# Optimization experiments

Hardware: AMD Instinct MI355X
Metric: run time of the kernel (lower is better)

The kernel has to match this reference:

```python
import jax, jax.numpy as jnp
import numpy as np

USER = 100000
ITEM = 200000
LATDIM = 128
GNN_LAYER = 3
UUGNN_LAYER = 2
N_EDGES = 600000
UU_EDGES = 300000


def setup_inputs() -> dict:
    key = jax.random.key(0)
    ks = jax.random.split(key, 8)
    N = USER + ITEM
    return {
        "uEmbeds0": jax.random.normal(ks[0], (USER, LATDIM), dtype=jnp.float32) * 0.05,
        "iEmbeds0": jax.random.normal(ks[1], (ITEM, LATDIM), dtype=jnp.float32) * 0.05,
        "adj_rows": jax.random.randint(ks[2], (N_EDGES,), 0, N, dtype=jnp.int32),
        "adj_cols": jax.random.randint(ks[3], (N_EDGES,), 0, N, dtype=jnp.int32),
        "adj_vals": jax.random.uniform(ks[4], (N_EDGES,), dtype=jnp.float32),
        "uadj_rows": jax.random.randint(ks[5], (UU_EDGES,), 0, USER, dtype=jnp.int32),
        "uadj_cols": jax.random.randint(ks[6], (UU_EDGES,), 0, USER, dtype=jnp.int32),
        "uadj_vals": jax.random.uniform(ks[7], (UU_EDGES,), dtype=jnp.float32),
    }


def _spmm(rows, cols, vals, x, n_rows):
    # out[r] = sum_{e: rows[e]==r} vals[e] * x[cols[e]]  (COO sparse @ dense)
    return jax.ops.segment_sum(vals[:, None] * x[cols], rows, num_segments=n_rows)


def reference(uEmbeds0, iEmbeds0, adj_rows, adj_cols, adj_vals,
              uadj_rows, uadj_cols, uadj_vals):
    N = USER + ITEM
    # LightGCN over bipartite adjacency, pool='sum' over layer-0..L embeddings
    # (dropout in eval mode -> identity)
    embeds = jnp.concatenate([uEmbeds0, iEmbeds0], axis=0)  # [N, d]
    acc = embeds
    for _ in range(GNN_LAYER):
        embeds = _spmm(adj_rows, adj_cols, adj_vals, embeds, N)
        acc = acc + embeds
    ui_uEmbed = acc[:USER]
    ui_iEmbed = acc[USER:]

    # LightGCN2 over user-user adjacency, sum of layer embeddings
    ulat = uEmbeds0
    uacc = ulat
    for _ in range(UUGNN_LAYER):
        ulat = _spmm(uadj_rows, uadj_cols, uadj_vals, ulat, USER)
        uacc = uacc + ulat
    return (ui_uEmbed, ui_iEmbed, uacc)
```

## Files before the change

### kernel.cpp

```cpp
#include <hip/hip_runtime.h>
#include <hip/hip_fp16.h>

#define USER_N   100000
#define ITEM_N   200000
#define LATDIM   128
#define NV4      32
#define NV8      16
#define N_TOTAL  300000
#define NR_ALL   400000
#define N_EDGES_C  600000
#define UU_EDGES_C 300000
#define NE_ALL   900000
#define SCAN_B   256
#define CONV_T   (N_TOTAL * NV8)

struct alignas(16) h8 { __half2 a, b, c, d; };
struct alignas(8)  Edge { int c; float v; };

typedef float f4_ext __attribute__((ext_vector_type(4)));
typedef int   i4_ext __attribute__((ext_vector_type(4)));
typedef int   i2_ext __attribute__((ext_vector_type(2)));

union H8I { i4_ext i; h8 h; };
union EDI { i2_ext i; Edge e; };

__device__ __forceinline__ float4 nt_load4(const float4* p) {
    f4_ext v = __builtin_nontemporal_load((const f4_ext*)p);
    return make_float4(v.x, v.y, v.z, v.w);
}
__device__ __forceinline__ void nt_store4(float4* p, float4 a) {
    f4_ext v = {a.x, a.y, a.z, a.w};
    __builtin_nontemporal_store(v, (f4_ext*)p);
}
__device__ __forceinline__ h8 nt_load_h8(const h8* p) {
    H8I u; u.i = __builtin_nontemporal_load((const i4_ext*)p);
    return u.h;
}
__device__ __forceinline__ Edge nt_load_edge(const Edge* p) {
    EDI u; u.i = __builtin_nontemporal_load((const i2_ext*)p);
    return u.e;
}

__device__ __forceinline__ h8 to_h8(float4 lo, float4 hi) {
    h8 r;
    r.a = __floats2half2_rn(lo.x, lo.y); r.b = __floats2half2_rn(lo.z, lo.w);
    r.c = __floats2half2_rn(hi.x, hi.y); r.d = __floats2half2_rn(hi.z, hi.w);
    return r;
}
__device__ __forceinline__ void h8_to_f(h8 h, float4& lo, float4& hi) {
    float2 p = __half22float2(h.a), q = __half22float2(h.b);
    float2 s = __half22float2(h.c), t = __half22float2(h.d);
    lo = make_float4(p.x, p.y, q.x, q.y);
    hi = make_float4(s.x, s.y, t.x, t.y);
}
__device__ __forceinline__ void fma4(float4& a, float v, float4 x) {
    a.x += v * x.x; a.y += v * x.y; a.z += v * x.z; a.w += v * x.w;
}
__device__ __forceinline__ float4 add4(float4 a, float4 b) {
    return make_float4(a.x + b.x, a.y + b.y, a.z + b.z, a.w + b.w);
}

__global__ void conv_hist_kernel(const float4* __restrict__ uE,
                                 const float4* __restrict__ iE,
                                 h8* __restrict__ E16,
                                 const int* __restrict__ ar,
                                 const int* __restrict__ ur,
                                 int* __restrict__ cnt) {
    int t = blockIdx.x * blockDim.x + threadIdx.x;
    if (t < CONV_T) {
        int f4i = t * 2;
        const int ub = USER_N * NV4;
        float4 lo, hi;
        if (f4i < ub) { lo = nt_load4(uE + f4i);        hi = nt_load4(uE + f4i + 1); }
        else          { lo = nt_load4(iE + (f4i - ub)); hi = nt_load4(iE + (f4i - ub) + 1); }
        E16[t] = to_h8(lo, hi);
    } else {
        int i = t - CONV_T;
        if (i < N_EDGES_C)   atomicAdd(&cnt[ar[i]], 1);
        else if (i < NE_ALL) atomicAdd(&cnt[ur[i - N_EDGES_C] + N_TOTAL], 1);
    }
}

__global__ void scan_block_kernel(const int* __restrict__ cnt,
                                  int* __restrict__ rptr,
                                  int* __restrict__ bsum, int n) {
    __shared__ int s[SCAN_B];
    int i = blockIdx.x * SCAN_B + threadIdx.x;
    int v = (i < n) ? cnt[i] : 0;
    s[threadIdx.x] = v;
    __syncthreads();
    for (int off = 1; off < SCAN_B; off <<= 1) {
        int t = (threadIdx.x >= off) ? s[threadIdx.x - off] : 0;
        __syncthreads();
        s[threadIdx.x] += t;
        __syncthreads();
    }
    if (i < n) rptr[i] = s[threadIdx.x] - v;
    if (threadIdx.x == SCAN_B - 1) bsum[blockIdx.x] = s[threadIdx.x];
}

__global__ void scan_bsum_kernel(int* __restrict__ bsum, int nb) {
    __shared__ int s[SCAN_B];
    __shared__ int carry;
    if (threadIdx.x == 0) carry = 0;
    __syncthreads();
    for (int base = 0; base < nb; base += SCAN_B) {
        int i = base + threadIdx.x;
        int v = (i < nb) ? bsum[i] : 0;
        s[threadIdx.x] = v;
        __syncthreads();
        for (int off = 1; off < SCAN_B; off <<= 1) {
            int t = (threadIdx.x >= off) ? s[threadIdx.x - off] : 0;
            __syncthreads();
            s[threadIdx.x] += t;
            __syncthreads();
        }
        if (i < nb) bsum[i] = s[threadIdx.x] - v + carry;
        __syncthreads();
        if (threadIdx.x == 0) carry += s[SCAN_B - 1];
        __syncthreads();
    }
}

__global__ void scan_add_kernel(int* __restrict__ rptr, const int* __restrict__ bsum,
                                int* __restrict__ cursor, int n, int n_edges) {
    int i = blockIdx.x * blockDim.x + threadIdx.x;
    if (i < n) {
        int v = rptr[i] + bsum[i / SCAN_B];
        rptr[i]   = v;
        cursor[i] = v;
    }
    if (i == 0) rptr[n] = n_edges;
}

__global__ void scatter2_kernel(const int* __restrict__ ar, const int* __restrict__ ac,
                                const float* __restrict__ av,
                                const int* __restrict__ ur, const int* __restrict__ uc,
                                const float* __restrict__ uv,
                                int* __restrict__ cursor,
                                Edge* __restrict__ edges) {
    int i = blockIdx.x * blockDim.x + threadIdx.x;
    int r; Edge ed;
    if (i < N_EDGES_C)      { r = ar[i];             ed.c = ac[i];           ed.v = av[i]; }
    else if (i < NE_ALL)    { int j = i - N_EDGES_C; r = ur[j] + N_TOTAL; ed.c = uc[j] + N_TOTAL; ed.v = uv[j]; }
    else return;
    int pos = atomicAdd(&cursor[r], 1);
    edges[pos] = ed;
}

__device__ __forceinline__ int e16_row(int c) {
    return (c < N_TOTAL) ? c : c - N_TOTAL;
}

__global__ void spmm_pass1(const int* __restrict__ rptr,
                           const Edge* __restrict__ edges,
                           const h8* __restrict__ E16,
                           h8* __restrict__ cur1) {
    int t = blockIdx.x * blockDim.x + threadIdx.x;
    int r = t >> 4, sub = t & 15;
    if (r >= NR_ALL) return;
    int e0 = rptr[r], e1 = rptr[r + 1];

    float4 a0l = make_float4(0,0,0,0), a0h = a0l, a1l = a0l, a1h = a0l;
    int e = e0;
    for (; e + 2 <= e1; e += 2) {
        Edge d0 = edges[e], d1 = edges[e + 1];
        h8 h0 = E16[(size_t)e16_row(d0.c) * NV8 + sub];
        h8 h1 = E16[(size_t)e16_row(d1.c) * NV8 + sub];
        float4 lo, hi;
        h8_to_f(h0, lo, hi); fma4(a0l, d0.v, lo); fma4(a0h, d0.v, hi);
        h8_to_f(h1, lo, hi); fma4(a1l, d1.v, lo); fma4(a1h, d1.v, hi);
    }
    if (e < e1) {
        Edge d0 = edges[e];
        h8 h0 = E16[(size_t)e16_row(d0.c) * NV8 + sub];
        float4 lo, hi;
        h8_to_f(h0, lo, hi); fma4(a0l, d0.v, lo); fma4(a0h, d0.v, hi);
    }
    cur1[(size_t)r * NV8 + sub] = to_h8(add4(a0l, a1l), add4(a0h, a1h));
}

__global__ void spmm_pass2(const int* __restrict__ rptr,
                           const Edge* __restrict__ edges,
                           const h8* __restrict__ cur1,
                           const h8* __restrict__ E16,
                           h8* __restrict__ cur2,
                           float4* __restrict__ uacc) {
    int t = blockIdx.x * blockDim.x + threadIdx.x;
    int r = t >> 4, sub = t & 15;
    if (r >= NR_ALL) return;
    int e0 = rptr[r], e1 = rptr[r + 1];

    float4 a0l = make_float4(0,0,0,0), a0h = a0l, a1l = a0l, a1h = a0l;
    int e = e0;
    for (; e + 2 <= e1; e += 2) {
        Edge d0 = edges[e], d1 = edges[e + 1];
        h8 h0 = cur1[(size_t)d0.c * NV8 + sub];
        h8 h1 = cur1[(size_t)d1.c * NV8 + sub];
        float4 lo, hi;
        h8_to_f(h0, lo, hi); fma4(a0l, d0.v, lo); fma4(a0h, d0.v, hi);
        h8_to_f(h1, lo, hi); fma4(a1l, d1.v, lo); fma4(a1h, d1.v, hi);
    }
    if (e < e1) {
        Edge d0 = edges[e];
        h8 h0 = cur1[(size_t)d0.c * NV8 + sub];
        float4 lo, hi;
        h8_to_f(h0, lo, hi); fma4(a0l, d0.v, lo); fma4(a0h, d0.v, hi);
    }
    float4 al = add4(a0l, a1l), ah = add4(a0h, a1h);

    size_t o = (size_t)r * NV8 + sub;
    if (r < N_TOTAL) {
        cur2[o] = to_h8(al, ah);
    } else {
        int ur = r - N_TOTAL;
        float4 u0l, u0h, l1l, l1h;
        h8_to_f(E16[(size_t)ur * NV8 + sub], u0l, u0h);
        h8_to_f(cur1[o], l1l, l1h);
        size_t of4 = (size_t)ur * NV4 + sub * 2;
        nt_store4(uacc + of4,     add4(add4(u0l, l1l), al));
        nt_store4(uacc + of4 + 1, add4(add4(u0h, l1h), ah));
    }
}

__global__ void spmm_pass3(const int* __restrict__ rptr,
                           const Edge* __restrict__ edges,
                           const h8* __restrict__ cur2,
                           const h8* __restrict__ cur1,
                           const h8* __restrict__ E16,
                           float4* __restrict__ acc) {
    int t = blockIdx.x * blockDim.x + threadIdx.x;
    int r = t >> 4, sub = t & 15;
    if (r >= N_TOTAL) return;
    int e0 = rptr[r], e1 = rptr[r + 1];

    float4 a0l = make_float4(0,0,0,0), a0h = a0l, a1l = a0l, a1h = a0l;
    int e = e0;
    for (; e + 2 <= e1; e += 2) {
        Edge d0 = nt_load_edge(edges + e), d1 = nt_load_edge(edges + e + 1);
        h8 h0 = cur2[(size_t)d0.c * NV8 + sub];
        h8 h1 = cur2[(size_t)d1.c * NV8 + sub];
        float4 lo, hi;
        h8_to_f(h0, lo, hi); fma4(a0l, d0.v, lo); fma4(a0h, d0.v, hi);
        h8_to_f(h1, lo, hi); fma4(a1l, d1.v, lo); fma4(a1h, d1.v, hi);
    }
    if (e < e1) {
        Edge d0 = nt_load_edge(edges + e);
        h8 h0 = cur2[(size_t)d0.c * NV8 + sub];
        float4 lo, hi;
        h8_to_f(h0, lo, hi); fma4(a0l, d0.v, lo); fma4(a0h, d0.v, hi);
    }
    float4 al = add4(a0l, a1l), ah = add4(a0h, a1h);

    size_t o = (size_t)r * NV8 + sub;
    float4 ezl, ezh, l1l, l1h, l2l, l2h;
    h8_to_f(nt_load_h8(E16 + o),  ezl, ezh);
    h8_to_f(nt_load_h8(cur1 + o), l1l, l1h);
    h8_to_f(cur2[o], l2l, l2h);

    size_t of4 = (size_t)r * NV4 + sub * 2;
    nt_store4(acc + of4,     add4(add4(ezl, l1l), add4(l2l, al)));
    nt_store4(acc + of4 + 1, add4(add4(ezh, l1h), add4(l2h, ah)));
}

extern "C" void kernel_launch(void* const* d_in, const int* in_sizes, int n_in,
                              void* d_out, int out_size, void* d_ws, size_t ws_size,
                              hipStream_t stream) {
    const float* uE    = (const float*)d_in[0];
    const float* iE    = (const float*)d_in[1];
    const int*   arows = (const int*)  d_in[2];
    const int*   acols = (const int*)  d_in[3];
    const float* avals = (const float*)d_in[4];
    const int*   urows = (const int*)  d_in[5];
    const int*   ucols = (const int*)  d_in[6];
    const float* uvals = (const float*)d_in[7];

    float* acc  = (float*)d_out;
    float* uacc = acc + (size_t)N_TOTAL * LATDIM;

    h8*    E16  = (h8*)d_ws;
    h8*    cur1 = E16 + (size_t)N_TOTAL * NV8;
    h8*    cur2 = cur1 + (size_t)NR_ALL * NV8;
    int*   cnt  = (int*)(cur2 + (size_t)N_TOTAL * NV8);
    int*   rptr = cnt + NR_ALL;
    int*   curp = rptr + NR_ALL + 1;
    int*   bsum = curp + NR_ALL;
    Edge*  edges = (Edge*)(bsum + 4096);

    const int TB = 256;

    hipMemsetAsync(cnt, 0, NR_ALL * sizeof(int), stream);
    {
        int threads = CONV_T + NE_ALL;
        conv_hist_kernel<<<(threads + TB - 1) / TB, TB, 0, stream>>>(
            (const float4*)uE, (const float4*)iE, E16, arows, urows, cnt);
    }
    {
        int nb = (NR_ALL + SCAN_B - 1) / SCAN_B;
        scan_block_kernel<<<nb, SCAN_B, 0, stream>>>(cnt, rptr, bsum, NR_ALL);
        scan_bsum_kernel<<<1, SCAN_B, 0, stream>>>(bsum, nb);
        scan_add_kernel<<<(NR_ALL + TB - 1) / TB, TB, 0, stream>>>(
            rptr, bsum, curp, NR_ALL, NE_ALL);
    }
    scatter2_kernel<<<(NE_ALL + TB - 1) / TB, TB, 0, stream>>>(
        arows, acols, avals, urows, ucols, uvals, curp, edges);

    {
        int threads = NR_ALL * NV8;
        int grid = (threads + TB - 1) / TB;
        spmm_pass1<<<grid, TB, 0, stream>>>(rptr, edges, E16, cur1);
        spmm_pass2<<<grid, TB, 0, stream>>>(rptr, edges, cur1, E16,
                                            cur2, (float4*)uacc);
    }
    {
        int threads = N_TOTAL * NV8;
        int grid = (threads + TB - 1) / TB;
        spmm_pass3<<<grid, TB, 0, stream>>>(rptr, edges, cur2, cur1, E16,
                                            (float4*)acc);
    }
}
```

Measured before the change: 352.8 us.

## Split fp32-to-fp16 conversion across hist, scan and scatter kernels

The embedding conversion to fp16 is divided into four chunks, and each chunk runs as extra blocks appended to the histogram, block-scan, scan-add and scatter kernels. This fills the latency-bound, low-occupancy CSR-build kernels with bandwidth work instead of doing all conversion up front. The spmm pass1 output store also becomes nontemporal. The cost is more complex kernels whose extra blocks may slow the critical atomic and scan phases.

```diff
diff --git a/kernel.cpp b/kernel.cpp
--- a/kernel.cpp
+++ b/kernel.cpp
@@ -13,6 +13,10 @@
 #define NE_ALL   900000
 #define SCAN_B   256
 #define CONV_T   (N_TOTAL * NV8)
+#define CONV_BLK 4688
+#define CONV_CS  (CONV_BLK * 256)
+#define HIST_BLK ((NE_ALL + 255) / 256)
+#define SCANB_BLK ((NR_ALL + SCAN_B - 1) / SCAN_B)
 
 struct alignas(16) h8 { __half2 a, b, c, d; };
 struct alignas(8)  Edge { int c; float v; };
@@ -35,6 +39,10 @@
 __device__ __forceinline__ h8 nt_load_h8(const h8* p) {
     H8I u; u.i = __builtin_nontemporal_load((const i4_ext*)p);
     return u.h;
+}
+__device__ __forceinline__ void nt_store_h8(h8* p, h8 v) {
+    H8I u; u.h = v;
+    __builtin_nontemporal_store(u.i, (i4_ext*)p);
 }
 __device__ __forceinline__ Edge nt_load_edge(const Edge* p) {
     EDI u; u.i = __builtin_nontemporal_load((const i2_ext*)p);
@@ -60,43 +68,53 @@
     return make_float4(a.x + b.x, a.y + b.y, a.z + b.z, a.w + b.w);
 }
 
-__global__ void conv_hist_kernel(const float4* __restrict__ uE,
-                                 const float4* __restrict__ iE,
-                                 h8* __restrict__ E16,
-                                 const int* __restrict__ ar,
-                                 const int* __restrict__ ur,
-                                 int* __restrict__ cnt) {
-    int t = blockIdx.x * blockDim.x + threadIdx.x;
-    if (t < CONV_T) {
-        int f4i = t * 2;
-        const int ub = USER_N * NV4;
-        float4 lo, hi;
-        if (f4i < ub) { lo = nt_load4(uE + f4i);        hi = nt_load4(uE + f4i + 1); }
-        else          { lo = nt_load4(iE + (f4i - ub)); hi = nt_load4(iE + (f4i - ub) + 1); }
-        E16[t] = to_h8(lo, hi);
-    } else {
-        int i = t - CONV_T;
+__device__ __forceinline__ void conv_do(int t, const float4* __restrict__ uE,
+                                        const float4* __restrict__ iE,
+                                        h8* __restrict__ E16) {
+    if (t < 0 || t >= CONV_T) return;
+    int f4i = t * 2;
+    const int ub = USER_N * NV4;
+    float4 lo, hi;
+    if (f4i < ub) { lo = nt_load4(uE + f4i);        hi = nt_load4(uE + f4i + 1); }
+    else          { lo = nt_load4(iE + (f4i - ub)); hi = nt_load4(iE + (f4i - ub) + 1); }
+    E16[t] = to_h8(lo, hi);
+}
+
+__global__ void hist_convA(const int* __restrict__ ar, const int* __restrict__ ur,
+                           int* __restrict__ cnt,
+                           const float4* __restrict__ uE, const float4* __restrict__ iE,
+                           h8* __restrict__ E16) {
+    if (blockIdx.x < HIST_BLK) {
+        int i = blockIdx.x * blockDim.x + threadIdx.x;
         if (i < N_EDGES_C)   atomicAdd(&cnt[ar[i]], 1);
         else if (i < NE_ALL) atomicAdd(&cnt[ur[i - N_EDGES_C] + N_TOTAL], 1);
-    }
-}
-
-__global__ void scan_block_kernel(const int* __restrict__ cnt,
-                                  int* __restrict__ rptr,
-                                  int* __restrict__ bsum, int n) {
-    __shared__ int s[SCAN_B];
-    int i = blockIdx.x * SCAN_B + threadIdx.x;
-    int v = (i < n) ? cnt[i] : 0;
-    s[threadIdx.x] = v;
-    __syncthreads();
-    for (int off = 1; off < SCAN_B; off <<= 1) {
-        int t = (threadIdx.x >= off) ? s[threadIdx.x - off] : 0;
+    } else {
+        conv_do((blockIdx.x - HIST_BLK) * 256 + (int)threadIdx.x, uE, iE, E16);
+    }
+}
+
+__global__ void scanblock_convB(const int* __restrict__ cnt,
+                                int* __restrict__ rptr, int* __restrict__ bsum,
+                                const float4* __restrict__ uE, const float4* __restrict__ iE,
+                                h8* __restrict__ E16) {
+    if (blockIdx.x < SCANB_BLK) {
+        __shared__ int s[SCAN_B];
+        int i = blockIdx.x * SCAN_B + threadIdx.x;
+        int v = (i < NR_ALL) ? cnt[i] : 0;
+        s[threadIdx.x] = v;
         __syncthreads();
-        s[threadIdx.x] += t;
-        __syncthreads();
-    }
-    if (i < n) rptr[i] = s[threadIdx.x] - v;
-    if (threadIdx.x == SCAN_B - 1) bsum[blockIdx.x] = s[threadIdx.x];
+        for (int off = 1; off < SCAN_B; off <<= 1) {
+            int t = (threadIdx.x >= off) ? s[threadIdx.x - off] : 0;
+            __syncthreads();
+            s[threadIdx.x] += t;
+            __syncthreads();
+        }
+        if (i < NR_ALL) rptr[i] = s[threadIdx.x] - v;
+        if (threadIdx.x == SCAN_B - 1) bsum[blockIdx.x] = s[threadIdx.x];
+    } else {
+        conv_do((blockIdx.x - SCANB_BLK) * 256 + (int)threadIdx.x + CONV_CS,
+                uE, iE, E16);
+    }
 }
 
 __global__ void scan_bsum_kernel(int* __restrict__ bsum, int nb) {
@@ -122,30 +140,43 @@
     }
 }
 
-__global__ void scan_add_kernel(int* __restrict__ rptr, const int* __restrict__ bsum,
-                                int* __restrict__ cursor, int n, int n_edges) {
-    int i = blockIdx.x * blockDim.x + threadIdx.x;
-    if (i < n) {
-        int v = rptr[i] + bsum[i / SCAN_B];
-        rptr[i]   = v;
-        cursor[i] = v;
-    }
-    if (i == 0) rptr[n] = n_edges;
-}
-
-__global__ void scatter2_kernel(const int* __restrict__ ar, const int* __restrict__ ac,
-                                const float* __restrict__ av,
-                                const int* __restrict__ ur, const int* __restrict__ uc,
-                                const float* __restrict__ uv,
-                                int* __restrict__ cursor,
-                                Edge* __restrict__ edges) {
-    int i = blockIdx.x * blockDim.x + threadIdx.x;
-    int r; Edge ed;
-    if (i < N_EDGES_C)      { r = ar[i];             ed.c = ac[i];           ed.v = av[i]; }
-    else if (i < NE_ALL)    { int j = i - N_EDGES_C; r = ur[j] + N_TOTAL; ed.c = uc[j] + N_TOTAL; ed.v = uv[j]; }
-    else return;
-    int pos = atomicAdd(&cursor[r], 1);
-    edges[pos] = ed;
+__global__ void scanadd_convC(int* __restrict__ rptr, const int* __restrict__ bsum,
+                              int* __restrict__ cursor,
+                              const float4* __restrict__ uE, const float4* __restrict__ iE,
+                              h8* __restrict__ E16) {
+    if (blockIdx.x < SCANB_BLK) {
+        int i = blockIdx.x * blockDim.x + threadIdx.x;
+        if (i < NR_ALL) {
+            int v = rptr[i] + bsum[i / SCAN_B];
+            rptr[i]   = v;
+            cursor[i] = v;
+        }
+        if (i == 0) rptr[NR_ALL] = NE_ALL;
+    } else {
+        conv_do((blockIdx.x - SCANB_BLK) * 256 + (int)threadIdx.x + 2 * CONV_CS,
+                uE, iE, E16);
+    }
+}
+
+__global__ void scatter_convD(const int* __restrict__ ar, const int* __restrict__ ac,
+                              const float* __restrict__ av,
+                              const int* __restrict__ ur, const int* __restrict__ uc,
+                              const float* __restrict__ uv,
+                              int* __restrict__ cursor, Edge* __restrict__ edges,
+                              const float4* __restrict__ uE, const float4* __restrict__ iE,
+                              h8* __restrict__ E16) {
+    if (blockIdx.x < HIST_BLK) {
+        int i = blockIdx.x * blockDim.x + threadIdx.x;
+        int r; Edge ed;
+        if (i < N_EDGES_C)   { r = ar[i];             ed.c = ac[i];           ed.v = av[i]; }
+        else if (i < NE_ALL) { int j = i - N_EDGES_C; r = ur[j] + N_TOTAL; ed.c = uc[j] + N_TOTAL; ed.v = uv[j]; }
+        else return;
+        int pos = atomicAdd(&cursor[r], 1);
+        edges[pos] = ed;
+    } else {
+        conv_do((blockIdx.x - HIST_BLK) * 256 + (int)threadIdx.x + 3 * CONV_CS,
+                uE, iE, E16);
+    }
 }
 
 __device__ __forceinline__ int e16_row(int c) {
@@ -177,7 +208,7 @@
         float4 lo, hi;
         h8_to_f(h0, lo, hi); fma4(a0l, d0.v, lo); fma4(a0h, d0.v, hi);
     }
-    cur1[(size_t)r * NV8 + sub] = to_h8(add4(a0l, a1l), add4(a0h, a1h));
+    nt_store_h8(cur1 + (size_t)r * NV8 + sub, to_h8(add4(a0l, a1l), add4(a0h, a1h)));
 }
 
 __global__ void spmm_pass2(const int* __restrict__ rptr,
@@ -288,22 +319,17 @@
     Edge*  edges = (Edge*)(bsum + 4096);
 
     const int TB = 256;
+    const float4* uE4 = (const float4*)uE;
+    const float4* iE4 = (const float4*)iE;
 
     hipMemsetAsync(cnt, 0, NR_ALL * sizeof(int), stream);
-    {
-        int threads = CONV_T + NE_ALL;
-        conv_hist_kernel<<<(threads + TB - 1) / TB, TB, 0, stream>>>(
-            (const float4*)uE, (const float4*)iE, E16, arows, urows, cnt);
-    }
-    {
-        int nb = (NR_ALL + SCAN_B - 1) / SCAN_B;
-        scan_block_kernel<<<nb, SCAN_B, 0, stream>>>(cnt, rptr, bsum, NR_ALL);
-        scan_bsum_kernel<<<1, SCAN_B, 0, stream>>>(bsum, nb);
-        scan_add_kernel<<<(NR_ALL + TB - 1) / TB, TB, 0, stream>>>(
-            rptr, bsum, curp, NR_ALL, NE_ALL);
-    }
-    scatter2_kernel<<<(NE_ALL + TB - 1) / TB, TB, 0, stream>>>(
-        arows, acols, avals, urows, ucols, uvals, curp, edges);
+
+    hist_convA<<<HIST_BLK + CONV_BLK, TB, 0, stream>>>(arows, urows, cnt, uE4, iE4, E16);
+    scanblock_convB<<<SCANB_BLK + CONV_BLK, SCAN_B, 0, stream>>>(cnt, rptr, bsum, uE4, iE4, E16);
+    scan_bsum_kernel<<<1, SCAN_B, 0, stream>>>(bsum, SCANB_BLK);
+    scanadd_convC<<<SCANB_BLK + CONV_BLK, TB, 0, stream>>>(rptr, bsum, curp, uE4, iE4, E16);
+    scatter_convD<<<HIST_BLK + CONV_BLK, TB, 0, stream>>>(
+        arows, acols, avals, urows, ucols, uvals, curp, edges, uE4, iE4, E16);
 
     {
         int threads = NR_ALL * NV8;
```

Result: slower. 364.4 us (+3.3%).

## Fuse CSR build and fp16 conversion into one cooperative kernel

Applied to the files above, without the earlier changes.

Replaces the memset, histogram/convert, three scan kernels and scatter kernel with a single cooperative kernel that uses grid-wide syncs between phases. The fp16 embedding conversion is split into quarters and interleaved with the histogram, block scan and bsum scan phases so that otherwise idle blocks have bandwidth work to do. This removes several kernel launches and their gaps. In exchange it adds five grid barriers, caps the grid at 1024 blocks with grid-stride loops, and depends on co-residency being possible under the launch bounds.

```diff
diff --git a/kernel.cpp b/kernel.cpp
--- a/kernel.cpp
+++ b/kernel.cpp
@@ -1,5 +1,8 @@
 #include <hip/hip_runtime.h>
 #include <hip/hip_fp16.h>
+#include <hip/hip_cooperative_groups.h>
+
+namespace cg = cooperative_groups;
 
 #define USER_N   100000
 #define ITEM_N   200000
@@ -13,6 +16,9 @@
 #define NE_ALL   900000
 #define SCAN_B   256
 #define CONV_T   (N_TOTAL * NV8)
+#define CONV_Q   (CONV_T / 4)
+#define NCH      ((NR_ALL + SCAN_B - 1) / SCAN_B)
+#define COOP_BLK 1024
 
 struct alignas(16) h8 { __half2 a, b, c, d; };
 struct alignas(8)  Edge { int c; float v; };
@@ -60,92 +66,105 @@
     return make_float4(a.x + b.x, a.y + b.y, a.z + b.z, a.w + b.w);
 }
 
-__global__ void conv_hist_kernel(const float4* __restrict__ uE,
-                                 const float4* __restrict__ iE,
-                                 h8* __restrict__ E16,
-                                 const int* __restrict__ ar,
-                                 const int* __restrict__ ur,
-                                 int* __restrict__ cnt) {
-    int t = blockIdx.x * blockDim.x + threadIdx.x;
-    if (t < CONV_T) {
-        int f4i = t * 2;
-        const int ub = USER_N * NV4;
-        float4 lo, hi;
-        if (f4i < ub) { lo = nt_load4(uE + f4i);        hi = nt_load4(uE + f4i + 1); }
-        else          { lo = nt_load4(iE + (f4i - ub)); hi = nt_load4(iE + (f4i - ub) + 1); }
-        E16[t] = to_h8(lo, hi);
-    } else {
-        int i = t - CONV_T;
-        if (i < N_EDGES_C)   atomicAdd(&cnt[ar[i]], 1);
-        else if (i < NE_ALL) atomicAdd(&cnt[ur[i - N_EDGES_C] + N_TOTAL], 1);
-    }
-}
-
-__global__ void scan_block_kernel(const int* __restrict__ cnt,
-                                  int* __restrict__ rptr,
-                                  int* __restrict__ bsum, int n) {
-    __shared__ int s[SCAN_B];
-    int i = blockIdx.x * SCAN_B + threadIdx.x;
-    int v = (i < n) ? cnt[i] : 0;
-    s[threadIdx.x] = v;
-    __syncthreads();
-    for (int off = 1; off < SCAN_B; off <<= 1) {
-        int t = (threadIdx.x >= off) ? s[threadIdx.x - off] : 0;
-        __syncthreads();
-        s[threadIdx.x] += t;
-        __syncthreads();
-    }
-    if (i < n) rptr[i] = s[threadIdx.x] - v;
-    if (threadIdx.x == SCAN_B - 1) bsum[blockIdx.x] = s[threadIdx.x];
-}
-
-__global__ void scan_bsum_kernel(int* __restrict__ bsum, int nb) {
+__device__ __forceinline__ void conv_do(int t, const float4* __restrict__ uE,
+                                        const float4* __restrict__ iE,
+                                        h8* __restrict__ E16) {
+    if (t < 0 || t >= CONV_T) return;
+    int f4i = t * 2;
+    const int ub = USER_N * NV4;
+    float4 lo, hi;
+    if (f4i < ub) { lo = nt_load4(uE + f4i);        hi = nt_load4(uE + f4i + 1); }
+    else          { lo = nt_load4(iE + (f4i - ub)); hi = nt_load4(iE + (f4i - ub) + 1); }
+    E16[t] = to_h8(lo, hi);
+}
+
+__global__ void __launch_bounds__(256, 4)
+csr_conv_coop(const float4* __restrict__ uE, const float4* __restrict__ iE,
+              h8* __restrict__ E16,
+              const int* __restrict__ ar, const int* __restrict__ ac,
+              const float* __restrict__ av,
+              const int* __restrict__ ur, const int* __restrict__ uc,
+              const float* __restrict__ uv,
+              int* __restrict__ cnt, int* __restrict__ rptr,
+              int* __restrict__ cursor, int* __restrict__ bsum,
+              Edge* __restrict__ edges) {
+    cg::grid_group grid = cg::this_grid();
     __shared__ int s[SCAN_B];
     __shared__ int carry;
-    if (threadIdx.x == 0) carry = 0;
-    __syncthreads();
-    for (int base = 0; base < nb; base += SCAN_B) {
-        int i = base + threadIdx.x;
-        int v = (i < nb) ? bsum[i] : 0;
+
+    const int NT  = COOP_BLK * 256;
+    const int tid = blockIdx.x * blockDim.x + threadIdx.x;
+
+    for (int i = tid; i < NR_ALL; i += NT) cnt[i] = 0;
+    for (int t = tid; t < CONV_Q; t += NT) conv_do(t, uE, iE, E16);
+    grid.sync();
+
+    for (int i = tid; i < NE_ALL; i += NT) {
+        if (i < N_EDGES_C) atomicAdd(&cnt[ar[i]], 1);
+        else               atomicAdd(&cnt[ur[i - N_EDGES_C] + N_TOTAL], 1);
+    }
+    for (int t = CONV_Q + tid; t < 2 * CONV_Q; t += NT) conv_do(t, uE, iE, E16);
+    grid.sync();
+
+    for (int ch = blockIdx.x; ch < NCH; ch += gridDim.x) {
+        int i = ch * SCAN_B + threadIdx.x;
+        int v = (i < NR_ALL) ? cnt[i] : 0;
         s[threadIdx.x] = v;
         __syncthreads();
         for (int off = 1; off < SCAN_B; off <<= 1) {
-            int t = (threadIdx.x >= off) ? s[threadIdx.x - off] : 0;
-            __syncthreads();
-            s[threadIdx.x] += t;
+            int t2 = (threadIdx.x >= off) ? s[threadIdx.x - off] : 0;
+            __syncthreads();
+            s[threadIdx.x] += t2;
             __syncthreads();
         }
-        if (i < nb) bsum[i] = s[threadIdx.x] - v + carry;
+        if (i < NR_ALL) rptr[i] = s[threadIdx.x] - v;
+        if (threadIdx.x == SCAN_B - 1) bsum[ch] = s[threadIdx.x];
         __syncthreads();
-        if (threadIdx.x == 0) carry += s[SCAN_B - 1];
+    }
+    for (int t = 2 * CONV_Q + tid; t < 3 * CONV_Q; t += NT) conv_do(t, uE, iE, E16);
+    grid.sync();
+
+    if (blockIdx.x == 0) {
+        if (threadIdx.x == 0) carry = 0;
         __syncthreads();
-    }
-}
-
-__global__ void scan_add_kernel(int* __restrict__ rptr, const int* __restrict__ bsum,
-                                int* __restrict__ cursor, int n, int n_edges) {
-    int i = blockIdx.x * blockDim.x + threadIdx.x;
-    if (i < n) {
+        for (int base = 0; base < NCH; base += SCAN_B) {
+            int i = base + threadIdx.x;
+            int v = (i < NCH) ? bsum[i] : 0;
+            s[threadIdx.x] = v;
+            __syncthreads();
+            for (int off = 1; off < SCAN_B; off <<= 1) {
+                int t2 = (threadIdx.x >= off) ? s[threadIdx.x - off] : 0;
+                __syncthreads();
+                s[threadIdx.x] += t2;
+                __syncthreads();
+            }
+            if (i < NCH) bsum[i] = s[threadIdx.x] - v + carry;
+            __syncthreads();
+            if (threadIdx.x == 0) carry += s[SCAN_B - 1];
+            __syncthreads();
+        }
+    } else {
+        int t = 3 * CONV_Q + (blockIdx.x - 1) * 256 + (int)threadIdx.x;
+        int stride = (COOP_BLK - 1) * 256;
+        for (; t < CONV_T; t += stride) conv_do(t, uE, iE, E16);
+    }
+    grid.sync();
+
+    for (int i = tid; i < NR_ALL; i += NT) {
         int v = rptr[i] + bsum[i / SCAN_B];
         rptr[i]   = v;
         cursor[i] = v;
     }
-    if (i == 0) rptr[n] = n_edges;
-}
-
-__global__ void scatter2_kernel(const int* __restrict__ ar, const int* __restrict__ ac,
-                                const float* __restrict__ av,
-                                const int* __restrict__ ur, const int* __restrict__ uc,
-                                const float* __restrict__ uv,
-                                int* __restrict__ cursor,
-                                Edge* __restrict__ edges) {
-    int i = blockIdx.x * blockDim.x + threadIdx.x;
-    int r; Edge ed;
-    if (i < N_EDGES_C)      { r = ar[i];             ed.c = ac[i];           ed.v = av[i]; }
-    else if (i < NE_ALL)    { int j = i - N_EDGES_C; r = ur[j] + N_TOTAL; ed.c = uc[j] + N_TOTAL; ed.v = uv[j]; }
-    else return;
-    int pos = atomicAdd(&cursor[r], 1);
-    edges[pos] = ed;
+    if (tid == 0) rptr[NR_ALL] = NE_ALL;
+    grid.sync();
+
+    for (int i = tid; i < NE_ALL; i += NT) {
+        int r; Edge ed;
+        if (i < N_EDGES_C) { r = ar[i];             ed.c = ac[i];           ed.v = av[i]; }
+        else               { int j = i - N_EDGES_C; r = ur[j] + N_TOTAL; ed.c = uc[j] + N_TOTAL; ed.v = uv[j]; }
+        int pos = atomicAdd(&cursor[r], 1);
+        edges[pos] = ed;
+    }
 }
 
 __device__ __forceinline__ int e16_row(int c) {
@@ -288,22 +307,19 @@
     Edge*  edges = (Edge*)(bsum + 4096);
 
     const int TB = 256;
-
-    hipMemsetAsync(cnt, 0, NR_ALL * sizeof(int), stream);
+    const float4* uE4 = (const float4*)uE;
+    const float4* iE4 = (const float4*)iE;
+
     {
-        int threads = CONV_T + NE_ALL;
-        conv_hist_kernel<<<(threads + TB - 1) / TB, TB, 0, stream>>>(
-            (const float4*)uE, (const float4*)iE, E16, arows, urows, cnt);
-    }
-    {
-        int nb = (NR_ALL + SCAN_B - 1) / SCAN_B;
-        scan_block_kernel<<<nb, SCAN_B, 0, stream>>>(cnt, rptr, bsum, NR_ALL);
-        scan_bsum_kernel<<<1, SCAN_B, 0, stream>>>(bsum, nb);
-        scan_add_kernel<<<(NR_ALL + TB - 1) / TB, TB, 0, stream>>>(
-            rptr, bsum, curp, NR_ALL, NE_ALL);
-    }
-    scatter2_kernel<<<(NE_ALL + TB - 1) / TB, TB, 0, stream>>>(
-        arows, acols, avals, urows, ucols, uvals, curp, edges);
+        void* params[] = {
+            (void*)&uE4, (void*)&iE4, (void*)&E16,
+            (void*)&arows, (void*)&acols, (void*)&avals,
+            (void*)&urows, (void*)&ucols, (void*)&uvals,
+            (void*)&cnt, (void*)&rptr, (void*)&curp, (void*)&bsum, (void*)&edges
+        };
+        hipLaunchCooperativeKernel((void*)csr_conv_coop,
+                                   dim3(COOP_BLK), dim3(TB), params, 0, stream);
+    }
 
     {
         int threads = NR_ALL * NV8;
```

New measurement: 930.8 us. +163.8%, slower.
